# Performance work log

Hardware: AMD Instinct MI355X
Metric: run time of the kernel (lower is better)

The kernel has to match this reference:

```python
import jax, jax.numpy as jnp
import numpy as np

MAX_SHIFT_BANDS = 2.0


def setup_inputs() -> dict:
    key = jax.random.key(0)
    k1, k2 = jax.random.split(key)
    B, Bh, H, W = 4, 128, 256, 256
    x = jax.random.normal(k1, (B, Bh, H, W), dtype=jnp.float32)
    wavelength_shift = jax.random.normal(k2, (B, Bh, W), dtype=jnp.float32)
    return {"x": x, "wavelength_shift": wavelength_shift}


def reference(x, wavelength_shift):
    # Faithful to torch grid_sample(mode='bilinear', padding_mode='border',
    # align_corners=False) applied along the spectral (band) axis only.
    B, Bh, H, W = x.shape
    dt = x.dtype

    shift = jnp.clip(wavelength_shift, -MAX_SHIFT_BANDS, MAX_SHIFT_BANDS)
    shift = shift[:, :, None, :]                         # [B,Bh,1,W]
    band = jnp.arange(Bh, dtype=dt)[None, :, None, None]  # [1,Bh,1,1]
    shifted = jnp.clip(band + shift, 0.0, Bh - 1)        # [B,Bh,1,W]

    # grid_sample align_corners=False unnormalization:
    # grid g = shifted/(Bh-1)*2 - 1 ; iy = ((g+1)*Bh - 1)/2 = shifted*Bh/(Bh-1) - 0.5
    iy = shifted * (Bh / (Bh - 1)) - 0.5                 # [B,Bh,1,W]
    i0f = jnp.floor(iy)
    w = iy - i0f                                          # lerp weight, [B,Bh,1,W]
    i0 = i0f.astype(jnp.int32)                            # may be -1 at low edge
    i0c = jnp.clip(i0, 0, Bh - 1)                         # border padding
    i1c = jnp.clip(i0 + 1, 0, Bh - 1)

    # broadcast gather indices over H rows
    i0c = jnp.broadcast_to(i0c, (B, Bh, H, W))
    i1c = jnp.broadcast_to(i1c, (B, Bh, H, W))

    x0 = jnp.take_along_axis(x, i0c, axis=1)              # [B,Bh,H,W]
    x1 = jnp.take_along_axis(x, i1c, axis=1)
    return x0 * (1.0 - w) + x1 * w
```

## Files before the change

### kernel.cpp

```cpp
#include <hip/hip_runtime.h>


#define BH_  128
#define H_   256
#define W_   256
#define TB    32
#define NLDS (TB + 6)

__global__ __launch_bounds__(512) void smile_kernel(
    const float* __restrict__ x,
    const float* __restrict__ ws,
    float* __restrict__ out)
{
    __shared__ float tile[NLDS][W_];

    const int t = threadIdx.x;
    int bid = blockIdx.x;
    const int tileI = bid & 3;
    bid >>= 2;
    const int h = bid & (H_ - 1);
    const int b = bid >> 8;
    const int bh0 = tileI * TB;

    const int wave = t >> 6;
    const int lane = t & 63;

    const float* __restrict__ xsrc = x + (size_t)b * (BH_ * H_ * W_) + h * W_;
    for (int i = wave; i < NLDS; i += 8) {
        const int band = min(max(bh0 - 3 + i, 0), BH_ - 1);
        const float* gp = xsrc + (size_t)band * (H_ * W_) + lane * 4;
        __builtin_amdgcn_global_load_lds(
            (const __attribute__((address_space(1))) void*)gp,
            (__attribute__((address_space(3))) void*)&tile[i][0],
            16, 0, 0);
    }

    const int bhbase = bh0 + wave * 4;
    const float* __restrict__ wsb = ws + (size_t)(b * BH_ + bhbase) * W_ + lane;
    float s[4][4];
#pragma unroll
    for (int r = 0; r < 4; ++r)
#pragma unroll
        for (int j = 0; j < 4; ++j)
            s[r][j] = wsb[r * W_ + j * 64];

    __syncthreads();

    const float scale = (float)(128.0 / 127.0);
    float* __restrict__ outp =
        out + (((size_t)b * BH_ + bhbase) * H_ + h) * W_ + lane;

#pragma unroll
    for (int r = 0; r < 4; ++r) {
        const int bh = bhbase + r;
#pragma unroll
        for (int j = 0; j < 4; ++j) {
            const int w = lane + j * 64;
            float sc      = fminf(fmaxf(s[r][j], -2.0f), 2.0f);
            float shifted = fminf(fmaxf((float)bh + sc, 0.0f), (float)(BH_ - 1));
            float iy      = fmaf(shifted, scale, -0.5f);
            float i0f     = floorf(iy);
            float frac    = iy - i0f;
            int   i0      = (int)i0f;
            int   r0      = min(max(i0, 0), BH_ - 1) - bh0 + 3;
            int   r1      = min(i0 + 1, BH_ - 1) - bh0 + 3;
            float x0 = tile[r0][w];
            float x1 = tile[r1][w];
            __builtin_nontemporal_store(
                fmaf(frac, x1 - x0, x0),
                outp + (size_t)r * (H_ * W_) + j * 64);
        }
    }
}

extern "C" void kernel_launch(void* const* d_in, const int* in_sizes, int n_in,
                              void* d_out, int out_size, void* d_ws, size_t ws_size,
                              hipStream_t stream) {
    const float* x  = (const float*)d_in[0];
    const float* ws = (const float*)d_in[1];
    float* out = (float*)d_out;

    const int grid = 4 * H_ * (BH_ / TB);
    smile_kernel<<<grid, 512, 0, stream>>>(x, ws, out);
}
```

Before: 47.63 us.

## Split tile load into two phases and overlap compute with second-half loads

Remaps block IDs with an XCD-style swizzle. Splits the LDS tile fill into a first batch of 22 rows and a second batch, so waves 0-3 can start computing after only the first batch lands while waves 4-7 wait for the rest. Replaces __syncthreads with manual vmcnt waits and s_barrier. The vmcnt counts are hand-tuned and risk being fragile if the compiler reorders or merges memory operations.

```diff
diff --git a/kernel.cpp b/kernel.cpp
--- a/kernel.cpp
+++ b/kernel.cpp
@@ -12,28 +12,35 @@
     const float* __restrict__ ws,
     float* __restrict__ out)
 {
-    __shared__ float tile[NLDS][W_];
+    __shared__ float tile[NLDS + 1][W_];
 
-    const int t = threadIdx.x;
-    int bid = blockIdx.x;
+    const int bid0 = blockIdx.x;
+    const int bid  = (bid0 & 7) * 512 + (bid0 >> 3);
+
     const int tileI = bid & 3;
-    bid >>= 2;
-    const int h = bid & (H_ - 1);
-    const int b = bid >> 8;
+    const int rem   = bid >> 2;
+    const int h   = rem & (H_ - 1);
+    const int b   = rem >> 8;
     const int bh0 = tileI * TB;
 
+    const int t    = threadIdx.x;
     const int wave = t >> 6;
     const int lane = t & 63;
 
     const float* __restrict__ xsrc = x + (size_t)b * (BH_ * H_ * W_) + h * W_;
-    for (int i = wave; i < NLDS; i += 8) {
-        const int band = min(max(bh0 - 3 + i, 0), BH_ - 1);
+
+#pragma unroll
+    for (int j = 0; j < 3; ++j) {
+        const int  i  = wave + j * 8;
+        const bool rl = (i < 22);
+        const int band = min(max(bh0 - 3 + (rl ? i : 0), 0), BH_ - 1);
         const float* gp = xsrc + (size_t)band * (H_ * W_) + lane * 4;
         __builtin_amdgcn_global_load_lds(
             (const __attribute__((address_space(1))) void*)gp,
-            (__attribute__((address_space(3))) void*)&tile[i][0],
+            (__attribute__((address_space(3))) void*)&tile[rl ? i : NLDS][0],
             16, 0, 0);
     }
+    __builtin_amdgcn_sched_barrier(0);
 
     const int bhbase = bh0 + wave * 4;
     const float* __restrict__ wsb = ws + (size_t)(b * BH_ + bhbase) * W_ + lane;
@@ -43,33 +50,67 @@
 #pragma unroll
         for (int j = 0; j < 4; ++j)
             s[r][j] = wsb[r * W_ + j * 64];
+    __builtin_amdgcn_sched_barrier(0);
 
-    __syncthreads();
+#pragma unroll
+    for (int j = 0; j < 2; ++j) {
+        const int i = 22 + wave + j * 8;
+        const int band = min(max(bh0 - 3 + i, 0), BH_ - 1);
+        const float* gp = xsrc + (size_t)band * (H_ * W_) + lane * 4;
+        __builtin_amdgcn_global_load_lds(
+            (const __attribute__((address_space(1))) void*)gp,
+            (__attribute__((address_space(3))) void*)&tile[i][0],
+            16, 0, 0);
+    }
+    __builtin_amdgcn_sched_barrier(0);
 
     const float scale = (float)(128.0 / 127.0);
     float* __restrict__ outp =
         out + (((size_t)b * BH_ + bhbase) * H_ + h) * W_ + lane;
 
+    auto COMPUTE = [&]() {
 #pragma unroll
-    for (int r = 0; r < 4; ++r) {
-        const int bh = bhbase + r;
+        for (int r = 0; r < 4; ++r) {
+            const int bh = bhbase + r;
 #pragma unroll
-        for (int j = 0; j < 4; ++j) {
-            const int w = lane + j * 64;
-            float sc      = fminf(fmaxf(s[r][j], -2.0f), 2.0f);
-            float shifted = fminf(fmaxf((float)bh + sc, 0.0f), (float)(BH_ - 1));
-            float iy      = fmaf(shifted, scale, -0.5f);
-            float i0f     = floorf(iy);
-            float frac    = iy - i0f;
-            int   i0      = (int)i0f;
-            int   r0      = min(max(i0, 0), BH_ - 1) - bh0 + 3;
-            int   r1      = min(i0 + 1, BH_ - 1) - bh0 + 3;
-            float x0 = tile[r0][w];
-            float x1 = tile[r1][w];
-            __builtin_nontemporal_store(
-                fmaf(frac, x1 - x0, x0),
-                outp + (size_t)r * (H_ * W_) + j * 64);
+            for (int j = 0; j < 4; ++j) {
+                const int w = lane + j * 64;
+                float sc      = fminf(fmaxf(s[r][j], -2.0f), 2.0f);
+                float shifted = fminf(fmaxf((float)bh + sc, 0.0f),
+                                      (float)(BH_ - 1));
+                float iy      = fmaf(shifted, scale, -0.5f);
+                float i0f     = floorf(iy);
+                float frac    = iy - i0f;
+                int   i0      = (int)i0f;
+                int   r0      = min(max(i0, 0), BH_ - 1) - bh0 + 3;
+                int   r1      = min(i0 + 1, BH_ - 1) - bh0 + 3;
+                float x0 = tile[r0][w];
+                float x1 = tile[r1][w];
+                __builtin_nontemporal_store(
+                    fmaf(frac, x1 - x0, x0),
+                    outp + (size_t)r * (H_ * W_) + j * 64);
+            }
         }
+    };
+
+    asm volatile("s_waitcnt vmcnt(2)" ::: "memory");
+    __builtin_amdgcn_s_barrier();
+    asm volatile("" ::: "memory");
+
+    if (wave < 4) {
+        COMPUTE();
+    }
+
+    if (wave < 4) {
+        asm volatile("s_waitcnt vmcnt(16)" ::: "memory");
+    } else {
+        asm volatile("s_waitcnt vmcnt(0)" ::: "memory");
+    }
+    __builtin_amdgcn_s_barrier();
+    asm volatile("" ::: "memory");
+
+    if (wave >= 4) {
+        COMPUTE();
     }
 }
 
```

Result: faster. 45.23 us (-5.0%).
